# Optimization experiments

Measured on AMD Instinct MI355X. Metric: run time of the kernel, lower is better.

## Reference

```python
import jax, jax.numpy as jnp
import numpy as np

DIM = 512
NUM_HEADS = 8
DIM_HEAD = 64
EPS = 1e-8
ROPE_THETA = 10000.0


def rms_norm(x, gamma):
    # F.normalize(x, dim=-1, p=2, eps) * sqrt(dim) * gamma
    norm = jnp.sqrt(jnp.sum(x * x, axis=-1, keepdims=True))
    x = x / jnp.maximum(norm, EPS)
    return x * (DIM ** 0.5) * gamma


def apply_rope(x):
    # x: [b, h, n, d], interleaved-pair RoPE (rotary-embedding-torch style)
    n, d = x.shape[-2], x.shape[-1]
    inv_freq = 1.0 / (ROPE_THETA ** (jnp.arange(0, d, 2, dtype=jnp.float32) / d))
    freqs = jnp.arange(n, dtype=jnp.float32)[:, None] * inv_freq[None, :]  # [n, d/2]
    freqs = jnp.repeat(freqs, 2, axis=-1)  # [n, d]
    cos, sin = jnp.cos(freqs), jnp.sin(freqs)
    x1 = x[..., ::2]
    x2 = x[..., 1::2]
    rot = jnp.stack((-x2, x1), axis=-1).reshape(x.shape)
    return x * cos + rot * sin


def setup_inputs() -> dict:
    key = jax.random.key(0)
    k1, k2, k3, k4 = jax.random.split(key, 4)
    b, n = 4, 2048
    dim_inner = NUM_HEADS * DIM_HEAD
    x = jax.random.normal(k1, (b, n, DIM), dtype=jnp.float32)
    gamma = jnp.ones((DIM,), dtype=jnp.float32)
    w_qkv = jax.random.normal(k2, (DIM, 3 * dim_inner), dtype=jnp.float32) * (DIM ** -0.5)
    w_out = jax.random.normal(k3, (dim_inner, DIM), dtype=jnp.float32) * (dim_inner ** -0.5)
    return {"x": x, "gamma": gamma, "w_qkv": w_qkv, "w_out": w_out}


def reference(x, gamma, w_qkv, w_out):
    b, n, _ = x.shape
    h, d = NUM_HEADS, DIM_HEAD
    xn = rms_norm(x, gamma)
    qkv = xn @ w_qkv  # [b, n, 3*h*d]
    qkv = qkv.reshape(b, n, 3, h, d)
    q = jnp.transpose(qkv[:, :, 0], (0, 2, 1, 3))  # [b, h, n, d]
    k = jnp.transpose(qkv[:, :, 1], (0, 2, 1, 3))
    v = jnp.transpose(qkv[:, :, 2], (0, 2, 1, 3))
    q = apply_rope(q)
    k = apply_rope(k)
    scale = d ** -0.5
    attn = jnp.einsum('bhnd,bhmd->bhnm', q, k) * scale
    attn = jax.nn.softmax(attn, axis=-1)
    out = jnp.einsum('bhnm,bhmd->bhnd', attn, v)
    out = jnp.transpose(out, (0, 2, 1, 3)).reshape(b, n, h * d)
    return out @ w_out
```

## Files before the change

### kernel.cpp

```cpp
#include <hip/hip_runtime.h>
#include <hip/hip_bf16.h>
#include <cmath>

#define B_SZ 4
#define N_SEQ 2048
#define DIM 512
#define NH 8
#define DH 64
#define QKV_N 1536
#define ROWS (B_SZ * N_SEQ)

typedef __bf16 bf16x8 __attribute__((ext_vector_type(8)));
typedef __bf16 bf16x4 __attribute__((ext_vector_type(4)));
typedef float  f32x4  __attribute__((ext_vector_type(4)));

#define GLOAD_LDS16(gp, lp)                                                     \
    __builtin_amdgcn_global_load_lds(                                           \
        (const __attribute__((address_space(1))) void*)(gp),                    \
        (__attribute__((address_space(3))) void*)(lp), 16, 0, 0)

#define MFMA_BF16 __builtin_amdgcn_mfma_f32_16x16x32_bf16

__global__ __launch_bounds__(64) void rmscast_kernel(const float* __restrict__ x,
                                                     const float* __restrict__ gamma,
                                                     __bf16* __restrict__ A) {
    int row = blockIdx.x;
    int t = threadIdx.x;
    const float4* xr = (const float4*)(x + (size_t)row * DIM);
    float4 a = xr[t];
    float4 b = xr[t + 64];
    float ss = a.x*a.x + a.y*a.y + a.z*a.z + a.w*a.w
             + b.x*b.x + b.y*b.y + b.z*b.z + b.w*b.w;
    #pragma unroll
    for (int off = 32; off > 0; off >>= 1) ss += __shfl_xor(ss, off, 64);
    float s = 22.62741699796952f / fmaxf(sqrtf(ss), 1e-8f);
    const float4* gr = (const float4*)gamma;
    float4 g1 = gr[t], g2 = gr[t + 64];
    bf16x4 o1 = { (__bf16)(a.x*g1.x*s), (__bf16)(a.y*g1.y*s),
                  (__bf16)(a.z*g1.z*s), (__bf16)(a.w*g1.w*s) };
    bf16x4 o2 = { (__bf16)(b.x*g2.x*s), (__bf16)(b.y*g2.y*s),
                  (__bf16)(b.z*g2.z*s), (__bf16)(b.w*g2.w*s) };
    *(bf16x4*)(A + (size_t)row * DIM + t * 4)       = o1;
    *(bf16x4*)(A + (size_t)row * DIM + 256 + t * 4) = o2;
}

__device__ __forceinline__ void tcast_tile(const float* __restrict__ W,
                                           __bf16* __restrict__ Wt,
                                           int K, int N, int n0, int k0, int t,
                                           float (*Ls)[68]) {
    const int tx = t & 15, ty = t >> 4;
    #pragma unroll
    for (int i = 0; i < 4; i++) {
        int k = ty + i * 16;
        float4 v = *(const float4*)&W[(size_t)(k0 + k) * N + n0 + tx * 4];
        *(float4*)&Ls[k][tx * 4] = v;
    }
    __syncthreads();
    const int nrow = t >> 2, seg = (t & 3) * 16;
    bf16x8 o0, o1;
    #pragma unroll
    for (int j = 0; j < 8; j++) o0[j] = (__bf16)Ls[seg + j][nrow];
    #pragma unroll
    for (int j = 0; j < 8; j++) o1[j] = (__bf16)Ls[seg + 8 + j][nrow];
    *(bf16x8*)&Wt[(size_t)(n0 + nrow) * K + k0 + seg]     = o0;
    *(bf16x8*)&Wt[(size_t)(n0 + nrow) * K + k0 + seg + 8] = o1;
}

__global__ __launch_bounds__(256) void tcast2_kernel(const float* __restrict__ w_qkv,
                                                     const float* __restrict__ w_out,
                                                     __bf16* __restrict__ Wqkvt,
                                                     __bf16* __restrict__ Woutt) {
    __shared__ float Ls[64][68];
    const int bx = blockIdx.x, k0 = blockIdx.y * 64, t = threadIdx.x;
    if (bx < 24) tcast_tile(w_qkv, Wqkvt, DIM, QKV_N, bx * 64, k0, t, Ls);
    else         tcast_tile(w_out, Woutt, DIM, DIM, (bx - 24) * 64, k0, t, Ls);
}

template <int N, typename OutT>
__global__ __launch_bounds__(256) void gemm_bf16_kernel(const __bf16* __restrict__ A,
                                                        const __bf16* __restrict__ Bt,
                                                        OutT* __restrict__ C) {
    __shared__ __bf16 As[128 * 32];
    __shared__ __bf16 Bs[128 * 32];
    const int t = threadIdx.x;
    const int lane = t & 63;
    const int w = t >> 6;
    const int l16 = lane & 15, quad = lane >> 4;
    const int wr = w >> 1, wc = w & 1;
    const int row0 = blockIdx.y * 128, col0 = blockIdx.x * 128;

    f32x4 acc[4][4] = {};

    const int r0a = t >> 2,         ks0 = (t & 3) * 8;
    const int r1a = (t + 256) >> 2, ks1 = (t & 3) * 8;

    for (int kt = 0; kt < DIM; kt += 32) {
        __syncthreads();
        GLOAD_LDS16(A  + (size_t)(row0 + r0a) * DIM + kt + ks0, As + t * 8);
        GLOAD_LDS16(A  + (size_t)(row0 + r1a) * DIM + kt + ks1, As + (t + 256) * 8);
        GLOAD_LDS16(Bt + (size_t)(col0 + r0a) * DIM + kt + ks0, Bs + t * 8);
        GLOAD_LDS16(Bt + (size_t)(col0 + r1a) * DIM + kt + ks1, Bs + (t + 256) * 8);
        __syncthreads();
        bf16x8 af[4], bfr[4];
        #pragma unroll
        for (int mi = 0; mi < 4; mi++)
            af[mi] = *(const bf16x8*)(As + (wr * 64 + mi * 16 + l16) * 32 + quad * 8);
        #pragma unroll
        for (int ni = 0; ni < 4; ni++)
            bfr[ni] = *(const bf16x8*)(Bs + (wc * 64 + ni * 16 + l16) * 32 + quad * 8);
        #pragma unroll
        for (int mi = 0; mi < 4; mi++)
            #pragma unroll
            for (int ni = 0; ni < 4; ni++)
                acc[mi][ni] = MFMA_BF16(af[mi], bfr[ni], acc[mi][ni], 0, 0, 0);
    }
    #pragma unroll
    for (int mi = 0; mi < 4; mi++) {
        #pragma unroll
        for (int ni = 0; ni < 4; ni++) {
            #pragma unroll
            for (int r = 0; r < 4; r++) {
                int m = row0 + wr * 64 + mi * 16 + quad * 4 + r;
                int n = col0 + wc * 64 + ni * 16 + l16;
                if constexpr (sizeof(OutT) == 4) {
                    C[(size_t)m * N + n] = acc[mi][ni][r];
                } else {
                    C[(size_t)m * N + n] = (__bf16)acc[mi][ni][r];
                }
            }
        }
    }
}

__global__ __launch_bounds__(256) void prep_kernel(const __bf16* __restrict__ qkvb,
                                                   __bf16* __restrict__ Qb,
                                                   __bf16* __restrict__ Kf,
                                                   __bf16* __restrict__ Vf) {
    const int bx = blockIdx.x;
    const int nt = bx & 31;
    const int bh = bx >> 5;
    const int b  = bh >> 3;
    const int h  = bh & 7;
    const int t  = threadIdx.x;
    const float QSCALE = 0.18033688011112042f;

    {
        const int r  = t >> 2;
        const int d0 = (t & 3) << 4;
        const int pos = nt * 64 + r;
        const __bf16* qp = qkvb + (size_t)(b * N_SEQ + pos) * QKV_N + h * DH + d0;

        union Pack { __bf16 h[16]; uint4 u[2]; };
        Pack qi, ki, qo, ko;
        qi.u[0] = ((const uint4*)qp)[0];         qi.u[1] = ((const uint4*)qp)[1];
        ki.u[0] = ((const uint4*)(qp + 512))[0]; ki.u[1] = ((const uint4*)(qp + 512))[1];

        #pragma unroll
        for (int i = 0; i < 8; i++) {
            int p = (d0 >> 1) + i;
            float inv = exp2f(-0.41524101186092028f * (float)p);
            float ang = (float)pos * inv;
            float sn, cs;
            sincosf(ang, &sn, &cs);
            float qe = (float)qi.h[2*i], qd = (float)qi.h[2*i+1];
            float ke = (float)ki.h[2*i], kd = (float)ki.h[2*i+1];
            qo.h[2*i]   = (__bf16)(QSCALE * (qe * cs - qd * sn));
            qo.h[2*i+1] = (__bf16)(QSCALE * (qd * cs + qe * sn));
            ko.h[2*i]   = (__bf16)(ke * cs - kd * sn);
            ko.h[2*i+1] = (__bf16)(kd * cs + ke * sn);
        }
        uint4* qd_ = (uint4*)(Qb + ((size_t)bh * N_SEQ + pos) * DH + d0);
        qd_[0] = qo.u[0]; qd_[1] = qo.u[1];
        const int group = r >> 4, kl = r & 15;
        const int c = d0 >> 5, quad = (d0 & 31) >> 3;
        __bf16* kdst = Kf + ((size_t)bh * 32 + nt) * 4096
                          + (group * 2 + c) * 512 + (quad * 16 + kl) * 8;
        *(uint4*)kdst         = ko.u[0];
        *(uint4*)(kdst + 128) = ko.u[1];
    }

    {
        const int w = t >> 6, lane = t & 63;
        union Pack { __bf16 h[16]; uint4 u[2]; };
        Pack v;
        #pragma unroll
        for (int j = 0; j < 16; j++) {
            int row = nt * 64 + w * 16 + j;
            v.h[j] = qkvb[(size_t)(b * N_SEQ + row) * QKV_N + 1024 + h * DH + lane];
        }
        const int ng = lane >> 4, vl = lane & 15;
        __bf16* vdst = Vf + ((size_t)bh * 32 + nt) * 4096
                          + (ng * 2 + (w >> 1)) * 512 + (((w & 1) * 2) * 16 + vl) * 8;
        *(uint4*)vdst         = v.u[0];
        *(uint4*)(vdst + 128) = v.u[1];
    }
}

__global__ __launch_bounds__(256, 2) void attn_mfma_kernel(const __bf16* __restrict__ Qb,
                                                           const __bf16* __restrict__ Kf,
                                                           const __bf16* __restrict__ Vf,
                                                           __bf16* __restrict__ attn) {
    __shared__ __bf16 kv[2][16384];
    __shared__ __bf16 plds[4][16][68];

    const int t    = threadIdx.x;
    const int w    = t >> 6;
    const int lane = t & 63;
    const int l16  = lane & 15;
    const int quad = lane >> 4;

    const int bx = blockIdx.x;
    const int bh = bx & 31;
    const int qc = bx >> 5;
    const int b  = bh >> 3;
    const int h  = bh & 7;

    const int qrow = qc * 128 + w * 32;
    const __bf16* Qh = Qb + ((size_t)bh * N_SEQ + qrow) * DH;
    const __bf16* Kt = Kf + (size_t)bh * 32 * 4096;
    const __bf16* Vt = Vf + (size_t)bh * 32 * 4096;

    bf16x8 qa[2][2];
    #pragma unroll
    for (int f = 0; f < 2; f++) {
        qa[f][0] = *(const bf16x8*)(Qh + (size_t)(f * 16 + l16) * DH + quad * 8);
        qa[f][1] = *(const bf16x8*)(Qh + (size_t)(f * 16 + l16) * DH + 32 + quad * 8);
    }

    bf16x8 ones;
    #pragma unroll
    for (int i = 0; i < 8; i++) ones[i] = (__bf16)1.0f;

    f32x4 O[2][4] = {};
    f32x4 L[2] = {};

    auto dma_tile = [&](int tt, int bb) {
        const __bf16* kss = Kt + (size_t)tt * 8192;
        const __bf16* vss = Vt + (size_t)tt * 8192;
        #pragma unroll
        for (int seg = 0; seg < 2; seg++) {
            GLOAD_LDS16(kss + seg * 4096 + w * 512 + lane * 8,
                        &kv[bb][seg * 4096 + w * 512 + lane * 8]);
            GLOAD_LDS16(kss + seg * 4096 + (w + 4) * 512 + lane * 8,
                        &kv[bb][seg * 4096 + (w + 4) * 512 + lane * 8]);
            GLOAD_LDS16(vss + seg * 4096 + w * 512 + lane * 8,
                        &kv[bb][8192 + seg * 4096 + w * 512 + lane * 8]);
            GLOAD_LDS16(vss + seg * 4096 + (w + 4) * 512 + lane * 8,
                        &kv[bb][8192 + seg * 4096 + (w + 4) * 512 + lane * 8]);
        }
    };

    dma_tile(0, 0);
    for (int tt = 0; tt < 16; tt++) {
        const int cur = tt & 1;
        __syncthreads();
        if (tt + 1 < 16) {
            dma_tile(tt + 1, cur ^ 1);
            asm volatile("s_waitcnt vmcnt(8)" ::: "memory");
        } else {
            asm volatile("s_waitcnt vmcnt(0)" ::: "memory");
        }
        __syncthreads();

        #pragma unroll
        for (int hh = 0; hh < 2; hh++) {
            const __bf16* kb = kv[cur] + hh * 4096;
            const __bf16* vb = kv[cur] + 8192 + hh * 4096;

            bf16x8 kf[4][2];
            #pragma unroll
            for (int g = 0; g < 4; g++)
                #pragma unroll
                for (int c = 0; c < 2; c++)
                    kf[g][c] = *(const bf16x8*)(kb + (g * 2 + c) * 512 + lane * 8);
            bf16x8 vf[4][2];
            #pragma unroll
            for (int n = 0; n < 4; n++)
                #pragma unroll
                for (int kc = 0; kc < 2; kc++)
                    vf[n][kc] = *(const bf16x8*)(vb + (n * 2 + kc) * 512 + lane * 8);

            #pragma unroll
            for (int f = 0; f < 2; f++) {
                f32x4 S[4];
                #pragma unroll
                for (int g = 0; g < 4; g++) {
                    f32x4 z = {0, 0, 0, 0};
                    z = MFMA_BF16(qa[f][0], kf[g][0], z, 0, 0, 0);
                    z = MFMA_BF16(qa[f][1], kf[g][1], z, 0, 0, 0);
                    S[g] = z;
                }
                #pragma unroll
                for (int g = 0; g < 4; g++)
                    #pragma unroll
                    for (int r = 0; r < 4; r++)
                        plds[w][quad * 4 + r][g * 16 + l16] =
                            (__bf16)__builtin_amdgcn_exp2f(S[g][r]);
                asm volatile("s_waitcnt lgkmcnt(0)" ::: "memory");
                bf16x8 pa0 = *(const bf16x8*)&plds[w][l16][quad * 8];
                bf16x8 pa1 = *(const bf16x8*)&plds[w][l16][32 + quad * 8];
                #pragma unroll
                for (int n = 0; n < 4; n++) {
                    O[f][n] = MFMA_BF16(pa0, vf[n][0], O[f][n], 0, 0, 0);
                    O[f][n] = MFMA_BF16(pa1, vf[n][1], O[f][n], 0, 0, 0);
                }
                L[f] = MFMA_BF16(pa0, ones, L[f], 0, 0, 0);
                L[f] = MFMA_BF16(pa1, ones, L[f], 0, 0, 0);
            }
        }
    }

    #pragma unroll
    for (int f = 0; f < 2; f++) {
        float inv[4];
        #pragma unroll
        for (int r = 0; r < 4; r++) inv[r] = 1.0f / L[f][r];
        #pragma unroll
        for (int n = 0; n < 4; n++)
            #pragma unroll
            for (int r = 0; r < 4; r++) {
                size_t row = (size_t)(b * N_SEQ + qrow + f * 16 + quad * 4 + r);
                attn[row * 512 + h * DH + n * 16 + l16] = (__bf16)(O[f][n][r] * inv[r]);
            }
    }
}

extern "C" void kernel_launch(void* const* d_in, const int* in_sizes, int n_in,
                              void* d_out, int out_size, void* d_ws, size_t ws_size,
                              hipStream_t stream) {
    const float* x     = (const float*)d_in[0];
    const float* gamma = (const float*)d_in[1];
    const float* w_qkv = (const float*)d_in[2];
    const float* w_out = (const float*)d_in[3];
    float* out = (float*)d_out;

    __bf16* Abf   = (__bf16*)d_ws;
    __bf16* Wqkvt = Abf + (size_t)ROWS * DIM;
    __bf16* Woutt = Wqkvt + (size_t)QKV_N * DIM;
    __bf16* qkvb  = Woutt + (size_t)DIM * DIM;
    __bf16* attnb = qkvb;
    __bf16* Qb    = qkvb + (size_t)ROWS * QKV_N;
    __bf16* Kf    = Qb + (size_t)NH * B_SZ * N_SEQ * DH;
    __bf16* Vf    = Kf + (size_t)NH * B_SZ * N_SEQ * DH;

    rmscast_kernel<<<ROWS, 64, 0, stream>>>(x, gamma, Abf);
    tcast2_kernel<<<dim3(32, 8), 256, 0, stream>>>(w_qkv, w_out, Wqkvt, Woutt);
    gemm_bf16_kernel<QKV_N, __bf16><<<dim3(QKV_N / 128, ROWS / 128), 256, 0, stream>>>(
        Abf, Wqkvt, qkvb);
    prep_kernel<<<1024, 256, 0, stream>>>(qkvb, Qb, Kf, Vf);
    attn_mfma_kernel<<<512, 256, 0, stream>>>(Qb, Kf, Vf, attnb);
    gemm_bf16_kernel<DIM, float><<<dim3(DIM / 128, ROWS / 128), 256, 0, stream>>>(
        attnb, Woutt, out);
}
```

Before: 175.7 us.

## Merge prelude kernels, shrink out-projection tiles, drop LDS wait in attention

Merges the RMS-norm cast and the weight transpose-cast into one launch, packing four rows per 256-thread block. Adds a dedicated out-projection GEMM with 64x128 tiles, which doubles the block count to 512 and fills more CUs. Removes an explicit lgkmcnt wait between the P writes to LDS and the reads back. That removal risks a read-after-write hazard unless the compiler inserts the wait itself.

Result: faster. 166.3 us (-5.4%).

```diff
diff --git a/kernel.cpp b/kernel.cpp
--- a/kernel.cpp
+++ b/kernel.cpp
@@ -21,29 +21,6 @@
 
 #define MFMA_BF16 __builtin_amdgcn_mfma_f32_16x16x32_bf16
 
-__global__ __launch_bounds__(64) void rmscast_kernel(const float* __restrict__ x,
-                                                     const float* __restrict__ gamma,
-                                                     __bf16* __restrict__ A) {
-    int row = blockIdx.x;
-    int t = threadIdx.x;
-    const float4* xr = (const float4*)(x + (size_t)row * DIM);
-    float4 a = xr[t];
-    float4 b = xr[t + 64];
-    float ss = a.x*a.x + a.y*a.y + a.z*a.z + a.w*a.w
-             + b.x*b.x + b.y*b.y + b.z*b.z + b.w*b.w;
-    #pragma unroll
-    for (int off = 32; off > 0; off >>= 1) ss += __shfl_xor(ss, off, 64);
-    float s = 22.62741699796952f / fmaxf(sqrtf(ss), 1e-8f);
-    const float4* gr = (const float4*)gamma;
-    float4 g1 = gr[t], g2 = gr[t + 64];
-    bf16x4 o1 = { (__bf16)(a.x*g1.x*s), (__bf16)(a.y*g1.y*s),
-                  (__bf16)(a.z*g1.z*s), (__bf16)(a.w*g1.w*s) };
-    bf16x4 o2 = { (__bf16)(b.x*g2.x*s), (__bf16)(b.y*g2.y*s),
-                  (__bf16)(b.z*g2.z*s), (__bf16)(b.w*g2.w*s) };
-    *(bf16x4*)(A + (size_t)row * DIM + t * 4)       = o1;
-    *(bf16x4*)(A + (size_t)row * DIM + 256 + t * 4) = o2;
-}
-
 __device__ __forceinline__ void tcast_tile(const float* __restrict__ W,
                                            __bf16* __restrict__ Wt,
                                            int K, int N, int n0, int k0, int t,
@@ -66,14 +43,40 @@
     *(bf16x8*)&Wt[(size_t)(n0 + nrow) * K + k0 + seg + 8] = o1;
 }
 
-__global__ __launch_bounds__(256) void tcast2_kernel(const float* __restrict__ w_qkv,
-                                                     const float* __restrict__ w_out,
-                                                     __bf16* __restrict__ Wqkvt,
-                                                     __bf16* __restrict__ Woutt) {
+__global__ __launch_bounds__(256) void prelude_kernel(const float* __restrict__ x,
+                                                      const float* __restrict__ gamma,
+                                                      const float* __restrict__ w_qkv,
+                                                      const float* __restrict__ w_out,
+                                                      __bf16* __restrict__ A,
+                                                      __bf16* __restrict__ Wqkvt,
+                                                      __bf16* __restrict__ Woutt) {
     __shared__ float Ls[64][68];
-    const int bx = blockIdx.x, k0 = blockIdx.y * 64, t = threadIdx.x;
-    if (bx < 24) tcast_tile(w_qkv, Wqkvt, DIM, QKV_N, bx * 64, k0, t, Ls);
-    else         tcast_tile(w_out, Woutt, DIM, DIM, (bx - 24) * 64, k0, t, Ls);
+    const int bx = blockIdx.x, t = threadIdx.x;
+    if (bx < 2048) {
+        const int row  = bx * 4 + (t >> 6);
+        const int lane = t & 63;
+        const float4* xr = (const float4*)(x + (size_t)row * DIM);
+        float4 a = xr[lane];
+        float4 b = xr[lane + 64];
+        float ss = a.x*a.x + a.y*a.y + a.z*a.z + a.w*a.w
+                 + b.x*b.x + b.y*b.y + b.z*b.z + b.w*b.w;
+        #pragma unroll
+        for (int off = 32; off > 0; off >>= 1) ss += __shfl_xor(ss, off, 64);
+        float s = 22.62741699796952f / fmaxf(sqrtf(ss), 1e-8f);
+        const float4* gr = (const float4*)gamma;
+        float4 g1 = gr[lane], g2 = gr[lane + 64];
+        bf16x4 o1 = { (__bf16)(a.x*g1.x*s), (__bf16)(a.y*g1.y*s),
+                      (__bf16)(a.z*g1.z*s), (__bf16)(a.w*g1.w*s) };
+        bf16x4 o2 = { (__bf16)(b.x*g2.x*s), (__bf16)(b.y*g2.y*s),
+                      (__bf16)(b.z*g2.z*s), (__bf16)(b.w*g2.w*s) };
+        *(bf16x4*)(A + (size_t)row * DIM + lane * 4)       = o1;
+        *(bf16x4*)(A + (size_t)row * DIM + 256 + lane * 4) = o2;
+    } else {
+        const int idx = bx - 2048;
+        const int k0 = (idx >> 5) * 64, c = idx & 31;
+        if (c < 24) tcast_tile(w_qkv, Wqkvt, DIM, QKV_N, c * 64, k0, t, Ls);
+        else        tcast_tile(w_out, Woutt, DIM, DIM, (c - 24) * 64, k0, t, Ls);
+    }
 }
 
 template <int N, typename OutT>
@@ -130,6 +133,54 @@
             }
         }
     }
+}
+
+__global__ __launch_bounds__(256) void gemm_out_kernel(const __bf16* __restrict__ A,
+                                                       const __bf16* __restrict__ Bt,
+                                                       float* __restrict__ C) {
+    __shared__ __bf16 As[64 * 32];
+    __shared__ __bf16 Bs[128 * 32];
+    const int t = threadIdx.x;
+    const int lane = t & 63;
+    const int w = t >> 6;
+    const int l16 = lane & 15, quad = lane >> 4;
+    const int wr = w >> 1, wc = w & 1;
+    const int row0 = blockIdx.y * 64, col0 = blockIdx.x * 128;
+
+    f32x4 acc[2][4] = {};
+
+    const int r0a = t >> 2, ks0 = (t & 3) * 8;
+    const int r1a = (t + 256) >> 2;
+
+    for (int kt = 0; kt < DIM; kt += 32) {
+        __syncthreads();
+        GLOAD_LDS16(A  + (size_t)(row0 + r0a) * DIM + kt + ks0, As + t * 8);
+        GLOAD_LDS16(Bt + (size_t)(col0 + r0a) * DIM + kt + ks0, Bs + t * 8);
+        GLOAD_LDS16(Bt + (size_t)(col0 + r1a) * DIM + kt + ks0, Bs + (t + 256) * 8);
+        __syncthreads();
+        bf16x8 af[2], bfr[4];
+        #pragma unroll
+        for (int mi = 0; mi < 2; mi++)
+            af[mi] = *(const bf16x8*)(As + (wr * 32 + mi * 16 + l16) * 32 + quad * 8);
+        #pragma unroll
+        for (int ni = 0; ni < 4; ni++)
+            bfr[ni] = *(const bf16x8*)(Bs + (wc * 64 + ni * 16 + l16) * 32 + quad * 8);
+        #pragma unroll
+        for (int mi = 0; mi < 2; mi++)
+            #pragma unroll
+            for (int ni = 0; ni < 4; ni++)
+                acc[mi][ni] = MFMA_BF16(af[mi], bfr[ni], acc[mi][ni], 0, 0, 0);
+    }
+    #pragma unroll
+    for (int mi = 0; mi < 2; mi++)
+        #pragma unroll
+        for (int ni = 0; ni < 4; ni++)
+            #pragma unroll
+            for (int r = 0; r < 4; r++) {
+                int m = row0 + wr * 32 + mi * 16 + quad * 4 + r;
+                int n = col0 + wc * 64 + ni * 16 + l16;
+                C[(size_t)m * 512 + n] = acc[mi][ni][r];
+            }
 }
 
 __global__ __launch_bounds__(256) void prep_kernel(const __bf16* __restrict__ qkvb,
@@ -296,7 +347,6 @@
                     for (int r = 0; r < 4; r++)
                         plds[w][quad * 4 + r][g * 16 + l16] =
                             (__bf16)__builtin_amdgcn_exp2f(S[g][r]);
-                asm volatile("s_waitcnt lgkmcnt(0)" ::: "memory");
                 bf16x8 pa0 = *(const bf16x8*)&plds[w][l16][quad * 8];
                 bf16x8 pa1 = *(const bf16x8*)&plds[w][l16][32 + quad * 8];
                 #pragma unroll
@@ -343,12 +393,11 @@
     __bf16* Kf    = Qb + (size_t)NH * B_SZ * N_SEQ * DH;
     __bf16* Vf    = Kf + (size_t)NH * B_SZ * N_SEQ * DH;
 
-    rmscast_kernel<<<ROWS, 64, 0, stream>>>(x, gamma, Abf);
-    tcast2_kernel<<<dim3(32, 8), 256, 0, stream>>>(w_qkv, w_out, Wqkvt, Woutt);
+    prelude_kernel<<<2304, 256, 0, stream>>>(x, gamma, w_qkv, w_out,
+                                             Abf, Wqkvt, Woutt);
     gemm_bf16_kernel<QKV_N, __bf16><<<dim3(QKV_N / 128, ROWS / 128), 256, 0, stream>>>(
         Abf, Wqkvt, qkvb);
     prep_kernel<<<1024, 256, 0, stream>>>(qkvb, Qb, Kf, Vf);
     attn_mfma_kernel<<<512, 256, 0, stream>>>(Qb, Kf, Vf, attnb);
-    gemm_bf16_kernel<DIM, float><<<dim3(DIM / 128, ROWS / 128), 256, 0, stream>>>(
-        attnb, Woutt, out);
-}
+    gemm_out_kernel<<<dim3(4, 128), 256, 0, stream>>>(attnb, Woutt, out);
+}
```
